# Kernel optimization log

Hardware: AMD Instinct MI355X
Metric: run time of the kernel (lower is better)

The kernel has to match this reference:

```python
import jax, jax.numpy as jnp
import numpy as np

B, F, DOF, N_CLS = 256, 1024, 64, 1000

def setup_inputs() -> dict:
    key = jax.random.key(0)
    k1, k2 = jax.random.split(key)
    x = jax.random.normal(k1, (B, F), dtype=jnp.float32)
    # min/max of the input domain, as the dataloader scan would estimate on randn data
    min_x = jnp.array([-3.0], dtype=jnp.float32)
    max_x = jnp.array([3.0], dtype=jnp.float32)
    W = jax.random.normal(k2, (N_CLS, F * DOF), dtype=jnp.float32) * 0.01
    return {"x": x, "min_x": min_x, "max_x": max_x, "W": W, "dof": DOF}


def _lagrange_embed(x, min_x, max_x, dof):
    # 1D P1 Lagrange basis. simplices[t] = (t+1, t), t = 0..dof-2.
    b_, f_ = x.shape
    T = dof - 1
    h = 1.0 / T  # uniform mesh spacing on [0, 1]
    # normalize to unit interval, flatten to scalar stream of length b = B*F
    xn = ((x.reshape(-1, 1) - min_x) / (max_x - min_x)).reshape(-1)  # (b,)
    t = jnp.arange(T, dtype=xn.dtype)                                 # (T,)
    s = xn[:, None] / h                                               # (b, T) broadcastable
    lam0 = s - t            # barycentric coord of vertex t+1  (b, T)
    lam1 = (t + 1.0) - s    # barycentric coord of vertex t    (b, T)
    n2t = ((lam0 >= 0.0) & (lam1 >= 0.0)).astype(xn.dtype)            # (b, T)
    z = jnp.zeros((xn.shape[0], 1), dtype=xn.dtype)
    # mask[b, p] = number of active simplices touching vertex p (scatter of n2t to p=t and p=t+1)
    mask = jnp.concatenate([n2t, z], axis=1) + jnp.concatenate([z, n2t], axis=1)  # (b, dof)
    # shape_values[b, p] = sum over active simplices of the barycentric value at vertex p
    w0 = n2t * lam0  # goes to vertex p = t+1
    w1 = n2t * lam1  # goes to vertex p = t
    shape_vals = jnp.concatenate([w1, z], axis=1) + jnp.concatenate([z, w0], axis=1)  # (b, dof)
    basis = shape_vals / jnp.maximum(mask, 1.0)
    # rescale back to the input domain (n_features == 1, so (1,) broadcasts)
    emb = basis * (max_x - min_x) + min_x  # (b, dof)
    return emb.reshape(b_, f_ * dof)


def reference(x, min_x, max_x, W, dof):
    emb = jax.lax.stop_gradient(_lagrange_embed(x, min_x, max_x, dof))  # .detach() in torch
    return emb @ W.T  # bias-free Linear: (B, n_cls)
```

## Files before the change

kernel.cpp:

```cpp
#include <hip/hip_runtime.h>
#include <cstdint>

#define NB 256
#define NF 1024
#define NDOF 64
#define NCLS 1000
#define CTILE 64
#define FGROUP 32
#define PSTR 65
#define BUFSZ 4168
#define BIAS_OFF (2 * BUFSZ)

__global__ __launch_bounds__(256) void lagr_meta(
    const float* __restrict__ x, const float* __restrict__ mnp,
    const float* __restrict__ mxp, float2* __restrict__ meta)
{
    __shared__ float2 tile[64][65];
    int f0 = blockIdx.x * 64;
    int b0 = blockIdx.y * 64;
    int tid = threadIdx.x;
    float mn = mnp[0], mx = mxp[0];
    float scale = mx - mn;

    int fl = tid & 63, br = tid >> 6;
#pragma unroll
    for (int i = 0; i < 16; ++i) {
        int bl = br + i * 4;
        float xv = x[(size_t)(b0 + bl) * NF + f0 + fl];
        float s = (xv - mn) / scale * 63.0f;
        float wA = 0.0f, wB = 0.0f;
        uint32_t t = 0u;
        if (s >= 0.0f && s <= 63.0f) {
            float tf = floorf(s);
            if (tf > 62.0f) tf = 62.0f;
            t  = (uint32_t)tf;
            wA = scale * (tf + 1.0f - s);
            wB = scale * (s - tf);
        }
        uint32_t bits = (__float_as_uint(wA) & ~63u) | t;
        tile[fl][bl] = make_float2(__uint_as_float(bits), wB);
    }
    __syncthreads();
    int bl = tid & 63, fr = tid >> 6;
#pragma unroll
    for (int i = 0; i < 16; ++i) {
        int f = fr + i * 4;
        meta[(size_t)(f0 + f) * NB + b0 + bl] = tile[f][bl];
    }
}

__global__ __launch_bounds__(512, 4) void lagr_main(
    const float2* __restrict__ meta, const float* __restrict__ W,
    const float* __restrict__ mnp, float* __restrict__ out)
{
    __shared__ float w_lds[2 * BUFSZ + 64];

    int tid  = threadIdx.x;
    int lane = tid & 63;
    int wave = tid >> 6;
    int c0 = blockIdx.y * CTILE;
    int f0 = blockIdx.x * FGROUP;

    int cst = tid >> 3;
    int q8  = tid & 7;
    int crow = c0 + cst;
    if (crow > NCLS - 1) crow = NCLS - 1;
    const float* wrow = W + (size_t)crow * (NF * NDOF);

    float acc[32];
#pragma unroll
    for (int i = 0; i < 32; ++i) acc[i] = 0.0f;
    float rowsum = 0.0f;
    int b0 = wave * 32;

    float4 st[2];
    auto issue = [&](int f) {
        const float4* src = (const float4*)(wrow + ((size_t)f << 6)) + (q8 << 1);
        st[0] = src[0];
        st[1] = src[1];
    };
    auto commit = [&](float* buf) {
        float* dst = buf + cst;
#pragma unroll
        for (int q = 0; q < 2; ++q) {
            int p = (q8 << 3) + (q << 2);
            rowsum += (st[q].x + st[q].y) + (st[q].z + st[q].w);
            dst[(p + 0) * PSTR] = st[q].x;
            dst[(p + 1) * PSTR] = st[q].y;
            dst[(p + 2) * PSTR] = st[q].z;
            dst[(p + 3) * PSTR] = st[q].w;
        }
    };

    float* cur = w_lds;
    float* nxt = w_lds + BUFSZ;

    issue(f0);
    commit(cur);
    __syncthreads();

#pragma unroll 1
    for (int ch = 0; ch < FGROUP; ++ch) {
        int f = f0 + ch;
        if (ch + 1 < FGROUP) issue(f + 1);

        float2 mreg = meta[(size_t)f * NB + b0 + (lane & 31)];
        const float* base = cur + lane;
#pragma unroll
        for (int j = 0; j < 32; ++j) {
            uint32_t mb = (uint32_t)__builtin_amdgcn_readlane(
                              (int)__float_as_uint(mreg.x), j);
            uint32_t wb = (uint32_t)__builtin_amdgcn_readlane(
                              (int)__float_as_uint(mreg.y), j);
            uint32_t t = mb & 63u;
            float a0 = base[t * PSTR];
            float a1 = base[t * PSTR + PSTR];
            acc[j] = fmaf(__uint_as_float(mb), a0,
                     fmaf(__uint_as_float(wb), a1, acc[j]));
        }

        if (ch + 1 < FGROUP) commit(nxt);
        float* tmp = cur; cur = nxt; nxt = tmp;
        __syncthreads();
    }

    rowsum += __shfl_xor(rowsum, 1);
    rowsum += __shfl_xor(rowsum, 2);
    rowsum += __shfl_xor(rowsum, 4);
    if (q8 == 0) w_lds[BIAS_OFF + cst] = mnp[0] * rowsum;
    __syncthreads();

    int c = c0 + lane;
    if (c < NCLS) {
        float bias = w_lds[BIAS_OFF + lane];
#pragma unroll
        for (int j = 0; j < 32; ++j) {
            atomicAdd(&out[(size_t)(b0 + j) * NCLS + c], acc[j] + bias);
        }
    }
}

extern "C" void kernel_launch(void* const* d_in, const int* in_sizes, int n_in,
                              void* d_out, int out_size, void* d_ws, size_t ws_size,
                              hipStream_t stream) {
    const float* x  = (const float*)d_in[0];
    const float* mn = (const float*)d_in[1];
    const float* mx = (const float*)d_in[2];
    const float* W  = (const float*)d_in[3];
    float* out = (float*)d_out;
    float2* meta = (float2*)d_ws;

    hipMemsetAsync(d_out, 0, (size_t)NB * NCLS * sizeof(float), stream);

    lagr_meta<<<dim3(NF / 64, NB / 64), dim3(256), 0, stream>>>(x, mn, mx, meta);

    dim3 grid(NF / FGROUP, (NCLS + CTILE - 1) / CTILE);
    lagr_main<<<grid, dim3(512), 0, stream>>>(meta, W, mn, out);
}
```

Baseline: 416.6 us.

## Replace gather-FMA inner loop with bf16 MFMA over one-hot Lagrange A fragments

Rewrites the main loop so that each feature's sparse two-nonzero basis row is built as a bf16 A fragment. The contraction against the W tile is then done with 32x32x16 bf16 MFMA instructions instead of per-row LDS gathers and scalar FMAs. The W tile is converted to bf16 and stored in a row-major LDS layout, which halves the LDS footprint, and the meta load is software-prefetched one step ahead. This trades fp32 accuracy in W and the basis weights for bf16, and spends most MFMA work on zeros from the mostly-zero A fragments.

New measurement: 408.6 us. About the same (-1.9%).

```diff
diff --git a/kernel.cpp b/kernel.cpp
--- a/kernel.cpp
+++ b/kernel.cpp
@@ -7,9 +7,15 @@
 #define NCLS 1000
 #define CTILE 64
 #define FGROUP 32
-#define PSTR 65
-#define BUFSZ 4168
-#define BIAS_OFF (2 * BUFSZ)
+#define ROWSTR 68
+
+typedef __attribute__((ext_vector_type(8))) short short8;
+typedef __attribute__((ext_vector_type(16))) float floatx16;
+
+static __device__ inline unsigned short f2bf(float f) {
+    uint32_t u = __float_as_uint(f);
+    return (unsigned short)((u + 0x7FFFu + ((u >> 16) & 1u)) >> 16);
+}
 
 __global__ __launch_bounds__(256) void lagr_meta(
     const float* __restrict__ x, const float* __restrict__ mnp,
@@ -53,11 +59,13 @@
     const float2* __restrict__ meta, const float* __restrict__ W,
     const float* __restrict__ mnp, float* __restrict__ out)
 {
-    __shared__ float w_lds[2 * BUFSZ + 64];
+    __shared__ unsigned short wt[2][64 * ROWSTR];
+    __shared__ float bias_s[64];
 
     int tid  = threadIdx.x;
     int lane = tid & 63;
     int wave = tid >> 6;
+    int half8 = (lane >> 5) << 3;
     int c0 = blockIdx.y * CTILE;
     int f0 = blockIdx.x * FGROUP;
 
@@ -67,11 +75,10 @@
     if (crow > NCLS - 1) crow = NCLS - 1;
     const float* wrow = W + (size_t)crow * (NF * NDOF);
 
-    float acc[32];
-#pragma unroll
-    for (int i = 0; i < 32; ++i) acc[i] = 0.0f;
+    floatx16 acc0, acc1;
+#pragma unroll
+    for (int r = 0; r < 16; ++r) { acc0[r] = 0.0f; acc1[r] = 0.0f; }
     float rowsum = 0.0f;
-    int b0 = wave * 32;
 
     float4 st[2];
     auto issue = [&](int f) {
@@ -79,21 +86,25 @@
         st[0] = src[0];
         st[1] = src[1];
     };
-    auto commit = [&](float* buf) {
-        float* dst = buf + cst;
-#pragma unroll
-        for (int q = 0; q < 2; ++q) {
-            int p = (q8 << 3) + (q << 2);
-            rowsum += (st[q].x + st[q].y) + (st[q].z + st[q].w);
-            dst[(p + 0) * PSTR] = st[q].x;
-            dst[(p + 1) * PSTR] = st[q].y;
-            dst[(p + 2) * PSTR] = st[q].z;
-            dst[(p + 3) * PSTR] = st[q].w;
-        }
+    auto commit = [&](unsigned short* buf) {
+        float v[8] = { st[0].x, st[0].y, st[0].z, st[0].w,
+                       st[1].x, st[1].y, st[1].z, st[1].w };
+        uint32_t d[4];
+#pragma unroll
+        for (int i = 0; i < 4; ++i) {
+            rowsum += v[2 * i] + v[2 * i + 1];
+            d[i] = (uint32_t)f2bf(v[2 * i]) | ((uint32_t)f2bf(v[2 * i + 1]) << 16);
+        }
+        unsigned short* dst = buf + cst * ROWSTR + (q8 << 3);
+        ((uint2*)dst)[0] = make_uint2(d[0], d[1]);
+        ((uint2*)dst)[1] = make_uint2(d[2], d[3]);
     };
 
-    float* cur = w_lds;
-    float* nxt = w_lds + BUFSZ;
+    unsigned short* cur = &wt[0][0];
+    unsigned short* nxt = &wt[1][0];
+
+    const float2* mbase = meta + wave * 32 + (lane & 31);
+    float2 mcur = mbase[(size_t)f0 * NB];
 
     issue(f0);
     commit(cur);
@@ -102,40 +113,74 @@
 #pragma unroll 1
     for (int ch = 0; ch < FGROUP; ++ch) {
         int f = f0 + ch;
-        if (ch + 1 < FGROUP) issue(f + 1);
-
-        float2 mreg = meta[(size_t)f * NB + b0 + (lane & 31)];
-        const float* base = cur + lane;
-#pragma unroll
-        for (int j = 0; j < 32; ++j) {
-            uint32_t mb = (uint32_t)__builtin_amdgcn_readlane(
-                              (int)__float_as_uint(mreg.x), j);
-            uint32_t wb = (uint32_t)__builtin_amdgcn_readlane(
-                              (int)__float_as_uint(mreg.y), j);
-            uint32_t t = mb & 63u;
-            float a0 = base[t * PSTR];
-            float a1 = base[t * PSTR + PSTR];
-            acc[j] = fmaf(__uint_as_float(mb), a0,
-                     fmaf(__uint_as_float(wb), a1, acc[j]));
-        }
-
-        if (ch + 1 < FGROUP) commit(nxt);
-        float* tmp = cur; cur = nxt; nxt = tmp;
+        bool more = (ch + 1 < FGROUP);
+        if (more) issue(f + 1);
+        float2 mnext = mcur;
+        if (more) mnext = mbase[(size_t)(f + 1) * NB];
+
+        uint32_t bits = __float_as_uint(mcur.x);
+        int t = (int)(bits & 63u);
+        uint32_t uA = f2bf(__uint_as_float(bits));
+        uint32_t uB = f2bf(mcur.y);
+        uint32_t P0 = uA | (uB << 16);
+        uint32_t P1 = uA << 16;
+        uint32_t P2 = uB;
+        short8 afrag[4];
+        int dbase = t - half8;
+#pragma unroll
+        for (int kc = 0; kc < 4; ++kc) {
+            union { uint32_t u[4]; short8 v; } a;
+#pragma unroll
+            for (int q = 0; q < 4; ++q) {
+                int e = dbase - kc * 16 - 2 * q;
+                a.u[q] = (e == 0) ? P0 : (e == 1) ? P1 : (e == -1) ? P2 : 0u;
+            }
+            afrag[kc] = a.v;
+        }
+
+        const unsigned short* rb = cur + (lane & 31) * ROWSTR + half8;
+#pragma unroll
+        for (int ct = 0; ct < 2; ++ct) {
+            const unsigned short* r = rb + ct * 32 * ROWSTR;
+#pragma unroll
+            for (int kc = 0; kc < 4; ++kc) {
+                union { uint2 u2[2]; short8 v; } bf;
+                bf.u2[0] = *(const uint2*)(r + kc * 16);
+                bf.u2[1] = *(const uint2*)(r + kc * 16 + 4);
+                if (ct == 0)
+                    acc0 = __builtin_amdgcn_mfma_f32_32x32x16_bf16(
+                               afrag[kc], bf.v, acc0, 0, 0, 0);
+                else
+                    acc1 = __builtin_amdgcn_mfma_f32_32x32x16_bf16(
+                               afrag[kc], bf.v, acc1, 0, 0, 0);
+            }
+        }
+
+        if (more) commit(nxt);
+        unsigned short* tmp = cur; cur = nxt; nxt = tmp;
+        mcur = mnext;
         __syncthreads();
     }
 
     rowsum += __shfl_xor(rowsum, 1);
     rowsum += __shfl_xor(rowsum, 2);
     rowsum += __shfl_xor(rowsum, 4);
-    if (q8 == 0) w_lds[BIAS_OFF + cst] = mnp[0] * rowsum;
+    if (q8 == 0) bias_s[cst] = mnp[0] * rowsum;
     __syncthreads();
 
-    int c = c0 + lane;
-    if (c < NCLS) {
-        float bias = w_lds[BIAS_OFF + lane];
-#pragma unroll
-        for (int j = 0; j < 32; ++j) {
-            atomicAdd(&out[(size_t)(b0 + j) * NCLS + c], acc[j] + bias);
+    int col = lane & 31;
+    int rowhi = (lane >> 5) << 2;
+#pragma unroll
+    for (int ct = 0; ct < 2; ++ct) {
+        int c = c0 + ct * 32 + col;
+        if (c < NCLS) {
+            float bias = bias_s[ct * 32 + col];
+            floatx16 a = ct ? acc1 : acc0;
+#pragma unroll
+            for (int r = 0; r < 16; ++r) {
+                int brow = (r & 3) + 8 * (r >> 2) + rowhi;
+                atomicAdd(&out[(size_t)(wave * 32 + brow) * NCLS + c], a[r] + bias);
+            }
         }
     }
 }
```
